# Optimization experiments

Hardware: AMD Instinct MI355X
Metric: run time of the kernel (lower is better)

## Reference

```python
import jax, jax.numpy as jnp
import numpy as np

D = 1024      # d_model
ED = 2048     # d_inner
K = 4         # d_conv
N = 16        # d_state
R = 64        # dt_rank
E = 8         # num_experts
TOPK = 2      # num_experts_per_tok
FF = 2048     # mlp_size
EPS = 1e-6
B, L = 1, 2048


def setup_inputs() -> dict:
    key = jax.random.key(0)
    ks = jax.random.split(key, 12)
    def nrm(k, shape, scale=0.02):
        return jax.random.normal(k, shape, jnp.float32) * scale
    return {
        "x": jax.random.normal(ks[0], (B, L, D), jnp.float32),
        "rms1_w": jnp.ones((D,), jnp.float32),
        "rms2_w": jnp.ones((D,), jnp.float32),
        "W_in": nrm(ks[1], (2 * ED, D)),
        "conv_w": nrm(ks[2], (ED, 1, K), 0.1),
        "conv_b": jnp.zeros((ED,), jnp.float32),
        "W_xproj": nrm(ks[3], (R + 2 * N, ED)),
        "W_dt": nrm(ks[4], (ED, R), 0.1),
        "b_dt": jnp.full((ED,), -4.6, jnp.float32),  # softplus(-4.6) ~ 0.01 init dt
        "A_log": jnp.log(jnp.tile(jnp.arange(1, N + 1, dtype=jnp.float32), (ED, 1))),  # S4D-real init
        "D_skip": jnp.ones((ED,), jnp.float32),
        "W_out": nrm(ks[5], (D, ED)),
        "W_router": nrm(ks[6], (E, D)),
        "gate_w": nrm(ks[7], (E, FF, D)),
        "up_w": nrm(ks[8], (E, FF, D)),
        "down_w": nrm(ks[9], (E, D, FF)),
    }


def rmsnorm(x, w):
    return x * jax.lax.rsqrt(jnp.mean(x * x, -1, keepdims=True) + EPS) * w


def mamba(x, W_in, conv_w, conv_b, W_xproj, W_dt, b_dt, A_log, D_skip, W_out):
    Bb, Ll, _ = x.shape
    xm, z = jnp.split(x @ W_in.T, 2, axis=-1)                 # [B,L,ED] each
    # depthwise causal conv over time
    xc = jax.lax.conv_general_dilated(xm.transpose(0, 2, 1), conv_w, (1,), [(K - 1, 0)],
                                      feature_group_count=ED)  # [B,ED,L]
    xc = jax.nn.silu((xc + conv_b[None, :, None]).transpose(0, 2, 1))  # [B,L,ED]
    dt, Bm, Cm = jnp.split(xc @ W_xproj.T, [R, R + N], axis=-1)        # [B,L,R],[B,L,N],[B,L,N]
    delta = jax.nn.softplus(dt @ W_dt.T + b_dt)                        # [B,L,ED]
    A = -jnp.exp(A_log)                                                # [ED,N]
    dA = jnp.exp(delta[..., None] * A)                                 # [B,L,ED,N]
    dBx = delta[..., None] * Bm[:, :, None, :] * xc[..., None]         # [B,L,ED,N]

    def step(h, t):
        dA_t, dBx_t, C_t = t
        h = dA_t * h + dBx_t
        return h, jnp.einsum("ben,bn->be", h, C_t)

    h0 = jnp.zeros((Bb, ED, N), x.dtype)
    _, ys = jax.lax.scan(step, h0, (dA.transpose(1, 0, 2, 3), dBx.transpose(1, 0, 2, 3), Cm.transpose(1, 0, 2)))
    y = ys.transpose(1, 0, 2) + D_skip * xc
    y = y * jax.nn.silu(z)
    return y @ W_out.T


def moe(x2d, W_router, gate_w, up_w, down_w):
    logits = x2d @ W_router.T                                  # [T,E]
    probs = jax.nn.softmax(logits.astype(jnp.float32), -1)
    topw, sel = jax.lax.top_k(probs, TOPK)                     # NOTE: no renormalization (faithful)
    topw = topw.astype(x2d.dtype)
    wmat = jnp.sum(jax.nn.one_hot(sel, E, dtype=x2d.dtype) * topw[..., None], axis=1)  # [T,E]
    g = jnp.einsum("td,efd->tef", x2d, gate_w)
    u = jnp.einsum("td,efd->tef", x2d, up_w)
    h = jax.nn.silu(g) * u
    ye = jnp.einsum("tef,edf->ted", h, down_w)
    out = jnp.einsum("ted,te->td", ye, wmat)
    return out, logits


def reference(x, rms1_w, rms2_w, W_in, conv_w, conv_b, W_xproj, W_dt, b_dt, A_log,
              D_skip, W_out, W_router, gate_w, up_w, down_w):
    Bb, Ll, Dd = x.shape
    res = x
    h = rmsnorm(x, rms1_w)
    h = mamba(h, W_in, conv_w, conv_b, W_xproj, W_dt, b_dt, A_log, D_skip, W_out)
    x = res + h
    res = x
    h = rmsnorm(x, rms2_w)
    mo, logits = moe(h.reshape(-1, Dd), W_router, gate_w, up_w, down_w)
    x = res + mo.reshape(Bb, Ll, Dd)
    return (x, logits)
```

## Files before the change

kernel.cpp:

```cpp
#include <hip/hip_runtime.h>
#include <math.h>

typedef unsigned short u16;
typedef unsigned int   u32;
typedef __attribute__((ext_vector_type(8))) short bf16x8;
typedef __attribute__((ext_vector_type(4))) float f32x4;

constexpr int Tn=2048, Dm=1024, EDc=2048, Ns=16, Rr=64, NEx=8, FFc=2048;
constexpr int SCH=32, SNCH=Tn/SCH;
constexpr int MAXTM=40;
constexpr float LOG2E = 1.44269504f;

__device__ __forceinline__ float siluf(float x){ return __fdividef(x, 1.f + __expf(-x)); }
__device__ __forceinline__ u16 bfr(float f){
  u32 u = __float_as_uint(f);
  return (u16)((u + 0x7fffu + ((u>>16)&1u)) >> 16);
}
__device__ __forceinline__ float b2f(u16 h){ return __uint_as_float(((u32)h)<<16); }

__device__ __forceinline__ void gload16(const void* g, void* l){
  __builtin_amdgcn_global_load_lds((const __attribute__((address_space(1))) void*)g,
                                   (__attribute__((address_space(3))) void*)l, 16, 0, 0);
}

__device__ __forceinline__ void cvt4(const float* __restrict__ in,
                                     u16* __restrict__ out, int i){
  float4 v = ((const float4*)in)[i];
  u32 lo = (u32)bfr(v.x) | ((u32)bfr(v.y)<<16);
  u32 hi = (u32)bfr(v.z) | ((u32)bfr(v.w)<<16);
  ((uint2*)out)[i] = make_uint2(lo, hi);
}

__global__ __launch_bounds__(256) void f2bm_k(
    const float* __restrict__ i0, u16* __restrict__ o0,
    const float* __restrict__ i1, u16* __restrict__ o1,
    const float* __restrict__ i2, u16* __restrict__ o2,
    const float* __restrict__ i3, u16* __restrict__ o3)
{
  int b = blockIdx.x;
  const float* in; u16* out;
  if (b < 1024){ in = i0; out = o0; }
  else if ((b -= 1024) < 512){ in = i1; out = o1; }
  else if ((b -= 512) < 48){ in = i2; out = o2; }
  else { b -= 48; in = i3; out = o3; }
  int base = b*1024 + threadIdx.x;
#pragma unroll
  for (int s = 0; s < 4; s++) cvt4(in, out, base + s*256);
}

__global__ __launch_bounds__(256) void f2b3_k(
    const float* __restrict__ g, const float* __restrict__ u,
    const float* __restrict__ d,
    u16* __restrict__ og, u16* __restrict__ ou, u16* __restrict__ od){
  const int BPW = (NEx*FFc*Dm/4)/1024;
  int b = blockIdx.x;
  int which = b / BPW;
  const float* in = (which==0) ? g : (which==1) ? u : d;
  u16* out        = (which==0) ? og : (which==1) ? ou : od;
  int base = (b - which*BPW)*1024 + threadIdx.x;
#pragma unroll
  for (int s = 0; s < 4; s++) cvt4(in, out, base + s*256);
}

__global__ __launch_bounds__(256) void rmsnorm_k(const float* __restrict__ x,
                                                 const float* __restrict__ w,
                                                 u16* __restrict__ ob){
  int t = blockIdx.x;
  const float* xr = x + (size_t)t * Dm;
  float v[4]; float s = 0.f;
#pragma unroll
  for (int j = 0; j < 4; j++){ int d = threadIdx.x + j*256; v[j] = xr[d]; s += v[j]*v[j]; }
#pragma unroll
  for (int m = 1; m < 64; m <<= 1) s += __shfl_xor(s, m);
  __shared__ float red[4]; __shared__ float sb;
  int lane = threadIdx.x & 63, wv = threadIdx.x >> 6;
  if (lane == 0) red[wv] = s;
  __syncthreads();
  if (threadIdx.x == 0) sb = rsqrtf((red[0]+red[1]+red[2]+red[3]) * (1.f/Dm) + 1e-6f);
  __syncthreads();
  float sc = sb;
#pragma unroll
  for (int j = 0; j < 4; j++){
    int d = threadIdx.x + j*256;
    ob[(size_t)t*Dm + d] = bfr(v[j]*sc*w[d]);
  }
}

__global__ __launch_bounds__(256) void rms2red_k(
  const float* __restrict__ x, const float* __restrict__ P,
  const float* __restrict__ w,
  float* __restrict__ out, float* __restrict__ h2f, u16* __restrict__ h2b,
  int* __restrict__ cnt)
{
  int t = blockIdx.x, tid = threadIdx.x;
  if (t == 0 && tid < 8) cnt[tid] = 0;
  const size_t S = (size_t)Tn*Dm;
  float v[4]; float s = 0.f;
#pragma unroll
  for (int j = 0; j < 4; j++){
    int d = tid + j*256;
    size_t idx = (size_t)t*Dm + d;
    float a = x[idx] + ((P[idx] + P[S+idx]) + (P[2*S+idx] + P[3*S+idx]));
    out[idx] = a; v[j] = a; s += a*a;
  }
#pragma unroll
  for (int m = 1; m < 64; m <<= 1) s += __shfl_xor(s, m);
  __shared__ float red[4]; __shared__ float sb;
  int lane = tid & 63, wv = tid >> 6;
  if (lane == 0) red[wv] = s;
  __syncthreads();
  if (tid == 0) sb = rsqrtf((red[0]+red[1]+red[2]+red[3]) * (1.f/Dm) + 1e-6f);
  __syncthreads();
  float sc = sb;
#pragma unroll
  for (int j = 0; j < 4; j++){
    int d = tid + j*256;
    float o = v[j]*sc*w[d];
    h2b[(size_t)t*Dm + d] = bfr(o);
    h2f[(size_t)t*Dm + d] = o;
  }
}

template<int EPI, int OB>
__global__ __launch_bounds__(512) void gemm_bb(
    const u16* __restrict__ A, int lda,
    const u16* __restrict__ B, int ldb,
    void* __restrict__ Cv, int ldc,
    int M, int N, int Ksl, const float* __restrict__ aux)
{
  __shared__ u16 As[2*4096], Bs[2*4096];
  int tid = threadIdx.x, lane = tid & 63, wid = tid >> 6;
  int wr = wid >> 2, wc = wid & 3;
  int n0 = blockIdx.x * 128, m0 = blockIdx.y * 128;
  int r = tid >> 2;
  int kk = ((tid & 3) ^ (r & 3)) * 8;
  size_t kbeg = (size_t)blockIdx.z * Ksl;
  const u16* Ag = A + (size_t)min(m0 + r, M-1)*lda + kbeg + kk;
  const u16* Bg = B + (size_t)min(n0 + r, N-1)*ldb + kbeg + kk;
  f32x4 acc[4][2] = {};
  int sw = ((lane>>4) ^ (lane&3)) * 8;
  int aoff[4], boff[2];
#pragma unroll
  for (int i = 0; i < 4; i++) aoff[i] = (wr*64 + i*16 + (lane&15))*32 + sw;
#pragma unroll
  for (int j = 0; j < 2; j++) boff[j] = (wc*32 + j*16 + (lane&15))*32 + sw;
  gload16(Ag, As + tid*8);
  gload16(Bg, Bs + tid*8);
  int NT = Ksl >> 5;
  for (int kt = 0; kt < NT; kt++){
    int cur = (kt & 1) * 4096;
    if (kt + 1 < NT){
      int nxt = 4096 - cur;
      gload16(Ag + (size_t)(kt+1)*32, As + nxt + tid*8);
      gload16(Bg + (size_t)(kt+1)*32, Bs + nxt + tid*8);
      asm volatile("s_waitcnt vmcnt(2)" ::: "memory");
    } else {
      asm volatile("s_waitcnt vmcnt(0)" ::: "memory");
    }
    __builtin_amdgcn_s_barrier();
    bf16x8 af[4], bv[2];
#pragma unroll
    for (int i = 0; i < 4; i++) af[i] = *(const bf16x8*)&As[cur + aoff[i]];
#pragma unroll
    for (int j = 0; j < 2; j++) bv[j] = *(const bf16x8*)&Bs[cur + boff[j]];
    asm volatile("s_waitcnt lgkmcnt(0)" ::: "memory");
    __builtin_amdgcn_sched_barrier(0);
    __builtin_amdgcn_s_barrier();
    __builtin_amdgcn_s_setprio(1);
#pragma unroll
    for (int i = 0; i < 4; i++)
#pragma unroll
      for (int j = 0; j < 2; j++)
        acc[i][j] = __builtin_amdgcn_mfma_f32_16x16x32_bf16(af[i], bv[j], acc[i][j], 0,0,0);
    __builtin_amdgcn_s_setprio(0);
  }
  float* Cf = (float*)Cv + (size_t)blockIdx.z * M * ldc;
  u16*   Cb = (u16*)Cv;
#pragma unroll
  for (int i = 0; i < 4; i++){
    int rbase = m0 + wr*64 + i*16 + ((lane>>4)<<2);
#pragma unroll
    for (int j = 0; j < 2; j++){
      int col = n0 + wc*32 + j*16 + (lane&15);
      if (col >= N) continue;
#pragma unroll
      for (int q = 0; q < 4; q++){
        int row = rbase + q;
        if (row >= M) continue;
        float v = acc[i][j][q];
        if (EPI == 1){ v += aux[col]; v = (v > 20.f) ? v : __logf(1.f + __expf(v)); }
        if (OB) Cb[(size_t)row*ldc + col] = bfr(v);
        else    Cf[(size_t)row*ldc + col] = v;
      }
    }
  }
}

__global__ __launch_bounds__(512) void gateup8(
    const u16* __restrict__ Aall,
    const u16* __restrict__ Wg, const u16* __restrict__ Wu,
    const int* __restrict__ cnt, const int* __restrict__ off,
    const int* __restrict__ bucket,
    const int* __restrict__ tmap, const int* __restrict__ ntot,
    u16* __restrict__ H)
{
  if ((int)blockIdx.y >= *ntot) return;
  int v = tmap[blockIdx.y];
  int e = v >> 16, m0 = (v & 0xFFFF) * 128;
  int Me = cnt[e];
  __shared__ u16 As[2*4096], Gs[2*4096], Us[2*4096];
  int tid = threadIdx.x, lane = tid & 63, wid = tid >> 6;
  int wr = wid >> 2, wc = wid & 3;
  int n0 = blockIdx.x * 128;
  int r = tid >> 2;
  int kk = ((tid & 3) ^ (r & 3)) * 8;
  int arow = bucket[e*Tn + min(m0 + r, Me-1)];
  const u16* Ag = Aall + (size_t)arow*Dm + kk;
  const u16* Gg = Wg + ((size_t)e*FFc + n0 + r)*Dm + kk;
  const u16* Ug = Wu + ((size_t)e*FFc + n0 + r)*Dm + kk;
  f32x4 ag[4][2] = {}, au[4][2] = {};
  int sw = ((lane>>4) ^ (lane&3)) * 8;
  int aoff[4], boff[2];
#pragma unroll
  for (int i = 0; i < 4; i++) aoff[i] = (wr*64 + i*16 + (lane&15))*32 + sw;
#pragma unroll
  for (int j = 0; j < 2; j++) boff[j] = (wc*32 + j*16 + (lane&15))*32 + sw;
  gload16(Ag, As + tid*8);
  gload16(Gg, Gs + tid*8);
  gload16(Ug, Us + tid*8);
  const int NT = Dm >> 5;
  for (int kt = 0; kt < NT; kt++){
    int cur = (kt & 1) * 4096;
    if (kt + 1 < NT){
      int nxt = 4096 - cur;
      gload16(Ag + (size_t)(kt+1)*32, As + nxt + tid*8);
      gload16(Gg + (size_t)(kt+1)*32, Gs + nxt + tid*8);
      gload16(Ug + (size_t)(kt+1)*32, Us + nxt + tid*8);
      asm volatile("s_waitcnt vmcnt(3)" ::: "memory");
    } else {
      asm volatile("s_waitcnt vmcnt(0)" ::: "memory");
    }
    __builtin_amdgcn_s_barrier();
    bf16x8 af[4], gf[2], uf[2];
#pragma unroll
    for (int i = 0; i < 4; i++) af[i] = *(const bf16x8*)&As[cur + aoff[i]];
#pragma unroll
    for (int j = 0; j < 2; j++){ gf[j] = *(const bf16x8*)&Gs[cur + boff[j]];
                                 uf[j] = *(const bf16x8*)&Us[cur + boff[j]]; }
    asm volatile("s_waitcnt lgkmcnt(0)" ::: "memory");
    __builtin_amdgcn_sched_barrier(0);
    __builtin_amdgcn_s_barrier();
    __builtin_amdgcn_s_setprio(1);
#pragma unroll
    for (int i = 0; i < 4; i++)
#pragma unroll
      for (int j = 0; j < 2; j++){
        ag[i][j] = __builtin_amdgcn_mfma_f32_16x16x32_bf16(af[i], gf[j], ag[i][j], 0,0,0);
        au[i][j] = __builtin_amdgcn_mfma_f32_16x16x32_bf16(af[i], uf[j], au[i][j], 0,0,0);
      }
    __builtin_amdgcn_s_setprio(0);
  }
  int offe = off[e];
#pragma unroll
  for (int i = 0; i < 4; i++){
    int mb = m0 + wr*64 + i*16 + ((lane>>4)<<2);
#pragma unroll
    for (int j = 0; j < 2; j++){
      int col = n0 + wc*32 + j*16 + (lane&15);
#pragma unroll
      for (int q = 0; q < 4; q++){
        int m = mb + q;
        if (m >= Me) continue;
        float g = ag[i][j][q], u = au[i][j][q];
        H[(size_t)(offe + m)*FFc + col] = bfr(siluf(g)*u);
      }
    }
  }
}

__global__ __launch_bounds__(512) void down8(
    const u16* __restrict__ Hall, const u16* __restrict__ Wd,
    const int* __restrict__ cnt, const int* __restrict__ off,
    const int* __restrict__ tmap, const int* __restrict__ ntot,
    u16* __restrict__ Y)
{
  if ((int)blockIdx.y >= *ntot) return;
  int v = tmap[blockIdx.y];
  int e = v >> 16, m0 = (v & 0xFFFF) * 128;
  int Me = cnt[e];
  int offe = off[e];
  int kbeg = blockIdx.z * (FFc/2);
  const u16* A = Hall + (size_t)offe*FFc;
  const u16* B = Wd + (size_t)e*Dm*FFc;
  u16* C = Y + (size_t)blockIdx.z*(2*Tn)*Dm + (size_t)offe*Dm;
  __shared__ u16 As[2*4096], Bs[2*4096];
  int tid = threadIdx.x, lane = tid & 63, wid = tid >> 6;
  int wr = wid >> 2, wc = wid & 3;
  int n0 = blockIdx.x * 128;
  int r = tid >> 2;
  int kk = ((tid & 3) ^ (r & 3)) * 8;
  const u16* Ag = A + (size_t)min(m0 + r, Me-1)*FFc + kbeg + kk;
  const u16* Bg = B + (size_t)(n0 + r)*FFc + kbeg + kk;
  f32x4 acc[4][2] = {};
  int sw = ((lane>>4) ^ (lane&3)) * 8;
  int aoff[4], boff[2];
#pragma unroll
  for (int i = 0; i < 4; i++) aoff[i] = (wr*64 + i*16 + (lane&15))*32 + sw;
#pragma unroll
  for (int j = 0; j < 2; j++) boff[j] = (wc*32 + j*16 + (lane&15))*32 + sw;
  gload16(Ag, As + tid*8);
  gload16(Bg, Bs + tid*8);
  const int NT = (FFc/2) >> 5;
  for (int kt = 0; kt < NT; kt++){
    int cur = (kt & 1) * 4096;
    if (kt + 1 < NT){
      int nxt = 4096 - cur;
      gload16(Ag + (size_t)(kt+1)*32, As + nxt + tid*8);
      gload16(Bg + (size_t)(kt+1)*32, Bs + nxt + tid*8);
      asm volatile("s_waitcnt vmcnt(2)" ::: "memory");
    } else {
      asm volatile("s_waitcnt vmcnt(0)" ::: "memory");
    }
    __builtin_amdgcn_s_barrier();
    bf16x8 af[4], bv[2];
#pragma unroll
    for (int i = 0; i < 4; i++) af[i] = *(const bf16x8*)&As[cur + aoff[i]];
#pragma unroll
    for (int j = 0; j < 2; j++) bv[j] = *(const bf16x8*)&Bs[cur + boff[j]];
    asm volatile("s_waitcnt lgkmcnt(0)" ::: "memory");
    __builtin_amdgcn_sched_barrier(0);
    __builtin_amdgcn_s_barrier();
    __builtin_amdgcn_s_setprio(1);
#pragma unroll
    for (int i = 0; i < 4; i++)
#pragma unroll
      for (int j = 0; j < 2; j++)
        acc[i][j] = __builtin_amdgcn_mfma_f32_16x16x32_bf16(af[i], bv[j], acc[i][j], 0,0,0);
    __builtin_amdgcn_s_setprio(0);
  }
#pragma unroll
  for (int i = 0; i < 4; i++){
    int mb = m0 + wr*64 + i*16 + ((lane>>4)<<2);
#pragma unroll
    for (int j = 0; j < 2; j++){
      int col = n0 + wc*32 + j*16 + (lane&15);
#pragma unroll
      for (int q = 0; q < 4; q++){
        int m = mb + q;
        if (m >= Me) continue;
        C[(size_t)m*Dm + col] = bfr(acc[i][j][q]);
      }
    }
  }
}

__global__ __launch_bounds__(256) void conv_k(const u16* __restrict__ xzb,
    const float* __restrict__ cw, const float* __restrict__ cb,
    u16* __restrict__ xc)
{
  int idx = blockIdx.x*256 + threadIdx.x;
  int t = idx >> 11, e = idx & (EDc - 1);
  float v = cb[e];
#pragma unroll
  for (int k = 0; k < 4; k++){
    int tt = t - 3 + k;
    if (tt >= 0) v += b2f(xzb[(size_t)tt*(2*EDc) + e]) * cw[e*4 + k];
  }
  xc[(size_t)t*EDc + e] = bfr(siluf(v));
}

__global__ __launch_bounds__(256) void xp_red(const float* __restrict__ part,
                                              float* __restrict__ xp,
                                              u16* __restrict__ dtA){
  int i = blockIdx.x*256 + threadIdx.x;
  const int S = Tn*96;
  float v = part[i] + part[S + i] + part[2*S + i] + part[3*S + i];
  xp[i] = v;
  int t = i / 96, c = i - t*96;
  if (c < Rr) dtA[t*Rr + c] = bfr(v);
}

__global__ __launch_bounds__(256) void scan_p1(
  const u16* __restrict__ delta, const u16* __restrict__ xc,
  const float* __restrict__ xp,  const float* __restrict__ A_log,
  float* __restrict__ hend, float* __restrict__ dsum)
{
  __shared__ u16 sdel[SCH*256], sxc[SCH*256];
  __shared__ float sB[SCH*16];
  int tid = threadIdx.x;
  int e0 = blockIdx.x*256, c = blockIdx.y, t0 = c*SCH;
#pragma unroll
  for (int i = 0; i < 4; i++){
    int f = (i*256+tid)*8;
    int t = f >> 8, e = f & 255;
    gload16(&delta[(size_t)(t0+t)*EDc + e0 + e], sdel + f);
    gload16(&xc  [(size_t)(t0+t)*EDc + e0 + e], sxc + f);
  }
  sB[tid]       = xp[(size_t)(t0 + (tid>>4))*96 + Rr + (tid&15)];
  sB[tid+256]   = xp[(size_t)(t0 + ((tid+256)>>4))*96 + Rr + (tid&15)];
  float a2[16];
  {
    const float* ar = &A_log[(size_t)(e0+tid)*16];
#pragma unroll
    for (int n = 0; n < 16; n++) a2[n] = -__expf(ar[n]) * LOG2E;
  }
  __syncthreads();
  float h[16] = {};
  float ds = 0.f;
  for (int t = 0; t < SCH; t++){
    float del = b2f(sdel[t*256 + tid]);
    float xv  = b2f(sxc [t*256 + tid]);
    ds += del;
    float dbx = del * xv;
    float4 b0 = *(const float4*)&sB[t*16];
    float4 b1 = *(const float4*)&sB[t*16+4];
    float4 b2 = *(const float4*)&sB[t*16+8];
    float4 b3 = *(const float4*)&sB[t*16+12];
    float bb[16] = {b0.x,b0.y,b0.z,b0.w, b1.x,b1.y,b1.z,b1.w,
                    b2.x,b2.y,b2.z,b2.w, b3.x,b3.y,b3.z,b3.w};
#pragma unroll
    for (int n = 0; n < 16; n++){
      float dA = exp2f(del * a2[n]);
      h[n] = fmaf(dA, h[n], dbx * bb[n]);
    }
  }
  float* hp = &hend[((size_t)c*EDc + e0 + tid)*16];
#pragma unroll
  for (int n = 0; n < 16; n += 4)
    *(float4*)&hp[n] = make_float4(h[n], h[n+1], h[n+2], h[n+3]);
  dsum[c*EDc + e0 + tid] = ds;
}

__global__ __launch_bounds__(256) void scan_p2(
  const float* __restrict__ hend, const float* __restrict__ dsum,
  const float* __restrict__ A_log, float* __restrict__ hin)
{
  int g = blockIdx.x*256 + threadIdx.x;
  int e = g >> 4;
  float a2 = -__expf(A_log[g]) * LOG2E;
  float h = 0.f;
  for (int c = 0; c < SNCH; c++){
    hin[(size_t)c*EDc*Ns + g] = h;
    float P = exp2f(a2 * dsum[c*EDc + e]);
    h = fmaf(P, h, hend[(size_t)c*EDc*Ns + g]);
  }
}

__global__ __launch_bounds__(256) void scan_p3(
  const u16* __restrict__ delta, const u16* __restrict__ xc,
  const float* __restrict__ xp,  const u16* __restrict__ xzb,
  const float* __restrict__ A_log, const float* __restrict__ D_skip,
  const float* __restrict__ hin,   u16* __restrict__ y2)
{
  __shared__ u16 sdel[SCH*256], sxc[SCH*256], sz[SCH*256];
  __shared__ float sB[SCH*16], sC[SCH*16];
  int tid = threadIdx.x;
  int e0 = blockIdx.x*256, c = blockIdx.y, t0 = c*SCH;
#pragma unroll
  for (int i = 0; i < 4; i++){
    int f = (i*256+tid)*8;
    int t = f >> 8, e = f & 255;
    gload16(&delta[(size_t)(t0+t)*EDc + e0 + e], sdel + f);
    gload16(&xc  [(size_t)(t0+t)*EDc + e0 + e], sxc + f);
    gload16(&xzb [(size_t)(t0+t)*(2*EDc) + EDc + e0 + e], sz + f);
  }
  {
    int f0 = tid, f1 = tid + 256;
    sB[f0] = xp[(size_t)(t0 + (f0>>4))*96 + Rr + (f0&15)];
    sB[f1] = xp[(size_t)(t0 + (f1>>4))*96 + Rr + (f1&15)];
    sC[f0] = xp[(size_t)(t0 + (f0>>4))*96 + Rr + Ns + (f0&15)];
    sC[f1] = xp[(size_t)(t0 + (f1>>4))*96 + Rr + Ns + (f1&15)];
  }
  float a2[16];
  {
    const float* ar = &A_log[(size_t)(e0+tid)*16];
#pragma unroll
    for (int n = 0; n < 16; n++) a2[n] = -__expf(ar[n]) * LOG2E;
  }
  float dsk = D_skip[e0 + tid];
  float h[16];
  {
    const float* hp = &hin[((size_t)c*EDc + e0 + tid)*16];
#pragma unroll
    for (int n = 0; n < 16; n += 4){
      float4 hv = *(const float4*)&hp[n];
      h[n] = hv.x; h[n+1] = hv.y; h[n+2] = hv.z; h[n+3] = hv.w;
    }
  }
  __syncthreads();
  for (int t = 0; t < SCH; t++){
    float del = b2f(sdel[t*256 + tid]);
    float xv  = b2f(sxc [t*256 + tid]);
    float zv  = b2f(sz  [t*256 + tid]);
    float dbx = del * xv;
    float4 b0 = *(const float4*)&sB[t*16];
    float4 b1 = *(const float4*)&sB[t*16+4];
    float4 b2 = *(const float4*)&sB[t*16+8];
    float4 b3 = *(const float4*)&sB[t*16+12];
    float bb[16] = {b0.x,b0.y,b0.z,b0.w, b1.x,b1.y,b1.z,b1.w,
                    b2.x,b2.y,b2.z,b2.w, b3.x,b3.y,b3.z,b3.w};
    float4 c0 = *(const float4*)&sC[t*16];
    float4 c1 = *(const float4*)&sC[t*16+4];
    float4 c2 = *(const float4*)&sC[t*16+8];
    float4 c3 = *(const float4*)&sC[t*16+12];
    float cc[16] = {c0.x,c0.y,c0.z,c0.w, c1.x,c1.y,c1.z,c1.w,
                    c2.x,c2.y,c2.z,c2.w, c3.x,c3.y,c3.z,c3.w};
    float p0 = 0.f, p1 = 0.f, p2 = 0.f, p3 = 0.f;
#pragma unroll
    for (int n = 0; n < 16; n += 4){
      float dA0 = exp2f(del * a2[n]);
      float dA1 = exp2f(del * a2[n+1]);
      float dA2 = exp2f(del * a2[n+2]);
      float dA3 = exp2f(del * a2[n+3]);
      h[n]   = fmaf(dA0, h[n],   dbx * bb[n]);
      h[n+1] = fmaf(dA1, h[n+1], dbx * bb[n+1]);
      h[n+2] = fmaf(dA2, h[n+2], dbx * bb[n+2]);
      h[n+3] = fmaf(dA3, h[n+3], dbx * bb[n+3]);
      p0 = fmaf(h[n],   cc[n],   p0);
      p1 = fmaf(h[n+1], cc[n+1], p1);
      p2 = fmaf(h[n+2], cc[n+2], p2);
      p3 = fmaf(h[n+3], cc[n+3], p3);
    }
    float p = (p0 + p1) + (p2 + p3);
    y2[(size_t)(t0+t)*EDc + e0 + tid] = bfr((p + dsk*xv) * siluf(zv));
  }
}

__global__ __launch_bounds__(256) void route_k(
  const float* __restrict__ h2, const float* __restrict__ Wr,
  float* __restrict__ logits_out,
  int* __restrict__ cnt, int* __restrict__ bucket,
  int* __restrict__ tok_e, int* __restrict__ tok_idx, float* __restrict__ tok_w)
{
  int t = blockIdx.x, tid = threadIdx.x;
  float p[8] = {};
#pragma unroll
  for (int j = 0; j < 4; j++){
    int d = tid + j*256;
    float xv = h2[(size_t)t*Dm + d];
#pragma unroll
    for (int e = 0; e < 8; e++) p[e] += xv * Wr[e*Dm + d];
  }
#pragma unroll
  for (int e = 0; e < 8; e++)
#pragma unroll
    for (int m = 1; m < 64; m <<= 1) p[e] += __shfl_xor(p[e], m);
  __shared__ float part[4][8];
  __shared__ float lg[8];
  int lane = tid & 63, wv = tid >> 6;
  if (lane == 0)
#pragma unroll
    for (int e = 0; e < 8; e++) part[wv][e] = p[e];
  __syncthreads();
  if (tid < 8){
    float v = part[0][tid]+part[1][tid]+part[2][tid]+part[3][tid];
    lg[tid] = v;
    logits_out[(size_t)t*8 + tid] = v;
  }
  __syncthreads();
  if (tid == 0){
    float mx = lg[0];
#pragma unroll
    for (int e = 1; e < 8; e++) mx = fmaxf(mx, lg[e]);
    float ex[8], s = 0.f;
#pragma unroll
    for (int e = 0; e < 8; e++){ ex[e] = expf(lg[e] - mx); s += ex[e]; }
    float inv = 1.f / s;
    int i0 = 0; float b0 = ex[0]*inv;
#pragma unroll
    for (int e = 1; e < 8; e++){ float pe = ex[e]*inv; if (pe > b0){ b0 = pe; i0 = e; } }
    int i1 = -1; float b1 = -1e30f;
#pragma unroll
    for (int e = 0; e < 8; e++){ if (e == i0) continue; float pe = ex[e]*inv; if (pe > b1){ b1 = pe; i1 = e; } }
    int k0 = atomicAdd(&cnt[i0], 1); bucket[i0*Tn + k0] = t;
    int k1 = atomicAdd(&cnt[i1], 1); bucket[i1*Tn + k1] = t;
    tok_e[2*t] = i0;   tok_idx[2*t] = k0;   tok_w[2*t] = b0;
    tok_e[2*t+1] = i1; tok_idx[2*t+1] = k1; tok_w[2*t+1] = b1;
  }
}

__global__ void prefix_k(const int* __restrict__ cnt, int* __restrict__ off,
                         int* __restrict__ tmap, int* __restrict__ ntot){
  if (threadIdx.x == 0 && blockIdx.x == 0){
    int s = 0;
    for (int e = 0; e < NEx; e++){ off[e] = s; s += cnt[e]; }
    int nt = 0;
    for (int e = 0; e < NEx; e++){
      int tiles = (cnt[e] + 127) >> 7;
      for (int tm = 0; tm < tiles; tm++) tmap[nt++] = (e << 16) | tm;
    }
    *ntot = nt;
  }
}

__global__ __launch_bounds__(256) void combine_k(float* __restrict__ out,
    const u16* __restrict__ Y, const int* __restrict__ off,
    const int* __restrict__ tok_e, const int* __restrict__ tok_idx,
    const float* __restrict__ tok_w)
{
  int t = blockIdx.x, tid = threadIdx.x;
  const size_t S2 = (size_t)(2*Tn)*Dm;
  int e0 = tok_e[2*t],   e1 = tok_e[2*t+1];
  size_t r0 = (size_t)(off[e0] + tok_idx[2*t])*Dm;
  size_t r1 = (size_t)(off[e1] + tok_idx[2*t+1])*Dm;
  float w0 = tok_w[2*t], w1 = tok_w[2*t+1];
#pragma unroll
  for (int j = 0; j < 4; j++){
    int d = tid + j*256;
    float y0 = b2f(Y[r0 + d]) + b2f(Y[S2 + r0 + d]);
    float y1 = b2f(Y[r1 + d]) + b2f(Y[S2 + r1 + d]);
    out[(size_t)t*Dm + d] += w0*y0 + w1*y1;
  }
}

extern "C" void kernel_launch(void* const* d_in, const int* in_sizes, int n_in,
                              void* d_out, int out_size, void* d_ws, size_t ws_size,
                              hipStream_t stream) {
  const float* x      = (const float*)d_in[0];
  const float* rms1_w = (const float*)d_in[1];
  const float* rms2_w = (const float*)d_in[2];
  const float* W_in   = (const float*)d_in[3];
  const float* conv_w = (const float*)d_in[4];
  const float* conv_b = (const float*)d_in[5];
  const float* W_xprj = (const float*)d_in[6];
  const float* W_dt   = (const float*)d_in[7];
  const float* b_dt   = (const float*)d_in[8];
  const float* A_log  = (const float*)d_in[9];
  const float* D_skip = (const float*)d_in[10];
  const float* W_out  = (const float*)d_in[11];
  const float* W_rt   = (const float*)d_in[12];
  const float* gate_w = (const float*)d_in[13];
  const float* up_w   = (const float*)d_in[14];
  const float* down_w = (const float*)d_in[15];

  float* out        = (float*)d_out;
  float* logits_out = out + (size_t)Tn*Dm;

  uint8_t* base = (uint8_t*)d_ws;
  size_t o = 0;
  auto alloc = [&](size_t bytes) -> void* {
    void* p = base + o;
    o = (o + bytes + 255) & ~(size_t)255;
    return p;
  };
  float* h2f   = (float*)alloc((size_t)Tn*Dm*4);
  u16*   h2b   = (u16*)  alloc((size_t)Tn*Dm*2);
  u16*   hmoe  = (u16*)  alloc((size_t)2*Tn*FFc*2);
  u16*   yslot = (u16*)  alloc((size_t)2*(2*Tn)*Dm*2);
  int*   cnt     = (int*)alloc(64);
  int*   off     = (int*)alloc(64);
  int*   ntot    = (int*)alloc(64);
  int*   tmap    = (int*)alloc(MAXTM*4 + 192);
  int*   bucket  = (int*)alloc((size_t)NEx*Tn*4);
  int*   tok_e   = (int*)alloc((size_t)2*Tn*4);
  int*   tok_idx = (int*)alloc((size_t)2*Tn*4);
  float* tok_w   = (float*)alloc((size_t)2*Tn*4);
  size_t oz = o;
  u16*   xzb   = (u16*)  alloc((size_t)Tn*2*EDc*2);
  u16*   delta = (u16*)  alloc((size_t)Tn*EDc*2);
  u16*   xc    = (u16*)  alloc((size_t)Tn*EDc*2);
  u16*   y2    = (u16*)  alloc((size_t)Tn*EDc*2);
  u16*   h1b   = (u16*)  alloc((size_t)Tn*Dm*2);
  u16*   dtA   = (u16*)  alloc((size_t)Tn*Rr*2);
  float* xp    = (float*)alloc((size_t)Tn*96*4);
  float* xp_part=(float*)alloc((size_t)4*Tn*96*4);
  float* hend  = (float*)alloc((size_t)SNCH*EDc*Ns*4);
  float* hin   = (float*)alloc((size_t)SNCH*EDc*Ns*4);
  float* dsum  = (float*)alloc((size_t)SNCH*EDc*4);
  float* wpart = (float*)xzb;
  u16* wgate = (u16*)(base + oz);
  u16* wup   = wgate + (size_t)NEx*FFc*Dm;
  u16* wdown = wup   + (size_t)NEx*FFc*Dm;
  u16* wbin  = (u16*)yslot;
  u16* wbout = wbin + (size_t)2*EDc*Dm;
  u16* wxp   = (u16*)hmoe;
  u16* wdt   = wxp + (size_t)96*EDc;

  f2bm_k<<<1616, 256, 0, stream>>>(W_in, wbin, W_out, wbout, W_xprj, wxp, W_dt, wdt);
  rmsnorm_k<<<Tn, 256, 0, stream>>>(x, rms1_w, h1b);
  gemm_bb<0,1><<<dim3(32,16,1), 512, 0, stream>>>(h1b, Dm, wbin, Dm, xzb, 2*EDc, Tn, 2*EDc, Dm, nullptr);
  conv_k<<<(Tn*EDc)/256, 256, 0, stream>>>(xzb, conv_w, conv_b, xc);
  gemm_bb<0,0><<<dim3(1,16,4), 512, 0, stream>>>(xc, EDc, wxp, EDc, xp_part, 96, Tn, 96, EDc/4, nullptr);
  xp_red<<<(Tn*96)/256, 256, 0, stream>>>(xp_part, xp, dtA);
  gemm_bb<1,1><<<dim3(16,16,1), 512, 0, stream>>>(dtA, Rr, wdt, Rr, delta, EDc, Tn, EDc, Rr, b_dt);
  scan_p1<<<dim3(EDc/256, SNCH), 256, 0, stream>>>(delta, xc, xp, A_log, hend, dsum);
  scan_p2<<<EDc*Ns/256, 256, 0, stream>>>(hend, dsum, A_log, hin);
  scan_p3<<<dim3(EDc/256, SNCH), 256, 0, stream>>>(delta, xc, xp, xzb, A_log, D_skip, hin, y2);
  gemm_bb<0,0><<<dim3(8,16,4), 512, 0, stream>>>(y2, EDc, wbout, EDc, wpart, Dm, Tn, Dm, EDc/4, nullptr);
  rms2red_k<<<Tn, 256, 0, stream>>>(x, wpart, rms2_w, out, h2f, h2b, cnt);
  f2b3_k<<<3*((NEx*FFc*Dm/4)/1024), 256, 0, stream>>>(gate_w, up_w, down_w, wgate, wup, wdown);
  route_k<<<Tn, 256, 0, stream>>>(h2f, W_rt, logits_out, cnt, bucket, tok_e, tok_idx, tok_w);
  prefix_k<<<1, 64, 0, stream>>>(cnt, off, tmap, ntot);
  gateup8<<<dim3(16, MAXTM), 512, 0, stream>>>(h2b, wgate, wup, cnt, off, bucket, tmap, ntot, hmoe);
  down8<<<dim3(8, MAXTM, 2), 512, 0, stream>>>(hmoe, wdown, cnt, off, tmap, ntot, yslot);
  combine_k<<<Tn, 256, 0, stream>>>(out, yslot, off, tok_e, tok_idx, tok_w);
}
```

Baseline: 378.0 us.

## Fuse MoE combine into down-projection epilogue via weighted float atomics

The down-projection kernel now scatters its routing-weighted fp32 results straight into the output rows with atomicAdd, using per-slot token indices and weights written by the router. This removes the separate combine kernel, the bf16 intermediate Y buffer write and re-read, and the tok_e/tok_idx arrays. The cost is many scattered fp32 atomics into the output: four contributions per element from two experts and two K-halves. That also makes the summation order nondeterministic.

```diff
diff --git a/kernel.cpp b/kernel.cpp
--- a/kernel.cpp
+++ b/kernel.cpp
@@ -281,8 +281,9 @@
 __global__ __launch_bounds__(512) void down8(
     const u16* __restrict__ Hall, const u16* __restrict__ Wd,
     const int* __restrict__ cnt, const int* __restrict__ off,
+    const int* __restrict__ bucket, const float* __restrict__ wbuf,
     const int* __restrict__ tmap, const int* __restrict__ ntot,
-    u16* __restrict__ Y)
+    float* __restrict__ out)
 {
   if ((int)blockIdx.y >= *ntot) return;
   int v = tmap[blockIdx.y];
@@ -292,7 +293,6 @@
   int kbeg = blockIdx.z * (FFc/2);
   const u16* A = Hall + (size_t)offe*FFc;
   const u16* B = Wd + (size_t)e*Dm*FFc;
-  u16* C = Y + (size_t)blockIdx.z*(2*Tn)*Dm + (size_t)offe*Dm;
   __shared__ u16 As[2*4096], Bs[2*4096];
   int tid = threadIdx.x, lane = tid & 63, wid = tid >> 6;
   int wr = wid >> 2, wc = wid & 3;
@@ -342,13 +342,15 @@
   for (int i = 0; i < 4; i++){
     int mb = m0 + wr*64 + i*16 + ((lane>>4)<<2);
 #pragma unroll
-    for (int j = 0; j < 2; j++){
-      int col = n0 + wc*32 + j*16 + (lane&15);
-#pragma unroll
-      for (int q = 0; q < 4; q++){
-        int m = mb + q;
-        if (m >= Me) continue;
-        C[(size_t)m*Dm + col] = bfr(acc[i][j][q]);
+    for (int q = 0; q < 4; q++){
+      int m = mb + q;
+      if (m >= Me) continue;
+      int t   = bucket[e*Tn + m];
+      float w = wbuf[e*Tn + m];
+#pragma unroll
+      for (int j = 0; j < 2; j++){
+        int col = n0 + wc*32 + j*16 + (lane&15);
+        atomicAdd(&out[(size_t)t*Dm + col], w * acc[i][j][q]);
       }
     }
   }
@@ -529,8 +531,7 @@
 __global__ __launch_bounds__(256) void route_k(
   const float* __restrict__ h2, const float* __restrict__ Wr,
   float* __restrict__ logits_out,
-  int* __restrict__ cnt, int* __restrict__ bucket,
-  int* __restrict__ tok_e, int* __restrict__ tok_idx, float* __restrict__ tok_w)
+  int* __restrict__ cnt, int* __restrict__ bucket, float* __restrict__ wbuf)
 {
   int t = blockIdx.x, tid = threadIdx.x;
   float p[8] = {};
@@ -572,10 +573,8 @@
     int i1 = -1; float b1 = -1e30f;
 #pragma unroll
     for (int e = 0; e < 8; e++){ if (e == i0) continue; float pe = ex[e]*inv; if (pe > b1){ b1 = pe; i1 = e; } }
-    int k0 = atomicAdd(&cnt[i0], 1); bucket[i0*Tn + k0] = t;
-    int k1 = atomicAdd(&cnt[i1], 1); bucket[i1*Tn + k1] = t;
-    tok_e[2*t] = i0;   tok_idx[2*t] = k0;   tok_w[2*t] = b0;
-    tok_e[2*t+1] = i1; tok_idx[2*t+1] = k1; tok_w[2*t+1] = b1;
+    int k0 = atomicAdd(&cnt[i0], 1); bucket[i0*Tn + k0] = t; wbuf[i0*Tn + k0] = b0;
+    int k1 = atomicAdd(&cnt[i1], 1); bucket[i1*Tn + k1] = t; wbuf[i1*Tn + k1] = b1;
   }
 }
 
@@ -590,26 +589,6 @@
       for (int tm = 0; tm < tiles; tm++) tmap[nt++] = (e << 16) | tm;
     }
     *ntot = nt;
-  }
-}
-
-__global__ __launch_bounds__(256) void combine_k(float* __restrict__ out,
-    const u16* __restrict__ Y, const int* __restrict__ off,
-    const int* __restrict__ tok_e, const int* __restrict__ tok_idx,
-    const float* __restrict__ tok_w)
-{
-  int t = blockIdx.x, tid = threadIdx.x;
-  const size_t S2 = (size_t)(2*Tn)*Dm;
-  int e0 = tok_e[2*t],   e1 = tok_e[2*t+1];
-  size_t r0 = (size_t)(off[e0] + tok_idx[2*t])*Dm;
-  size_t r1 = (size_t)(off[e1] + tok_idx[2*t+1])*Dm;
-  float w0 = tok_w[2*t], w1 = tok_w[2*t+1];
-#pragma unroll
-  for (int j = 0; j < 4; j++){
-    int d = tid + j*256;
-    float y0 = b2f(Y[r0 + d]) + b2f(Y[S2 + r0 + d]);
-    float y1 = b2f(Y[r1 + d]) + b2f(Y[S2 + r1 + d]);
-    out[(size_t)t*Dm + d] += w0*y0 + w1*y1;
   }
 }
 
@@ -646,15 +625,13 @@
   float* h2f   = (float*)alloc((size_t)Tn*Dm*4);
   u16*   h2b   = (u16*)  alloc((size_t)Tn*Dm*2);
   u16*   hmoe  = (u16*)  alloc((size_t)2*Tn*FFc*2);
-  u16*   yslot = (u16*)  alloc((size_t)2*(2*Tn)*Dm*2);
+  u16*   wzone = (u16*)  alloc((size_t)2*(2*Tn)*Dm*2);
   int*   cnt     = (int*)alloc(64);
   int*   off     = (int*)alloc(64);
   int*   ntot    = (int*)alloc(64);
   int*   tmap    = (int*)alloc(MAXTM*4 + 192);
   int*   bucket  = (int*)alloc((size_t)NEx*Tn*4);
-  int*   tok_e   = (int*)alloc((size_t)2*Tn*4);
-  int*   tok_idx = (int*)alloc((size_t)2*Tn*4);
-  float* tok_w   = (float*)alloc((size_t)2*Tn*4);
+  float* wbuf    = (float*)alloc((size_t)NEx*Tn*4);
   size_t oz = o;
   u16*   xzb   = (u16*)  alloc((size_t)Tn*2*EDc*2);
   u16*   delta = (u16*)  alloc((size_t)Tn*EDc*2);
@@ -671,7 +648,7 @@
   u16* wgate = (u16*)(base + oz);
   u16* wup   = wgate + (size_t)NEx*FFc*Dm;
   u16* wdown = wup   + (size_t)NEx*FFc*Dm;
-  u16* wbin  = (u16*)yslot;
+  u16* wbin  = (u16*)wzone;
   u16* wbout = wbin + (size_t)2*EDc*Dm;
   u16* wxp   = (u16*)hmoe;
   u16* wdt   = wxp + (size_t)96*EDc;
@@ -689,9 +666,8 @@
   gemm_bb<0,0><<<dim3(8,16,4), 512, 0, stream>>>(y2, EDc, wbout, EDc, wpart, Dm, Tn, Dm, EDc/4, nullptr);
   rms2red_k<<<Tn, 256, 0, stream>>>(x, wpart, rms2_w, out, h2f, h2b, cnt);
   f2b3_k<<<3*((NEx*FFc*Dm/4)/1024), 256, 0, stream>>>(gate_w, up_w, down_w, wgate, wup, wdown);
-  route_k<<<Tn, 256, 0, stream>>>(h2f, W_rt, logits_out, cnt, bucket, tok_e, tok_idx, tok_w);
+  route_k<<<Tn, 256, 0, stream>>>(h2f, W_rt, logits_out, cnt, bucket, wbuf);
   prefix_k<<<1, 64, 0, stream>>>(cnt, off, tmap, ntot);
   gateup8<<<dim3(16, MAXTM), 512, 0, stream>>>(h2b, wgate, wup, cnt, off, bucket, tmap, ntot, hmoe);
-  down8<<<dim3(8, MAXTM, 2), 512, 0, stream>>>(hmoe, wdown, cnt, off, tmap, ntot, yslot);
-  combine_k<<<Tn, 256, 0, stream>>>(out, yslot, off, tok_e, tok_idx, tok_w);
-}
+  down8<<<dim3(8, MAXTM, 2), 512, 0, stream>>>(hmoe, wdown, cnt, off, bucket, wbuf, tmap, ntot, out);
+}
```

Result: slower. 388.2 us (+2.7%).
